# Kernel optimization log

Measured on AMD Instinct MI355X. Metric: run time of the kernel, lower is better.

## Reference

```python
import jax, jax.numpy as jnp
import numpy as np

T, B, IN, HID, OUT = 100, 2048, 784, 100, 10
BETA = 0.9      # snn.Leaky(beta=0.9)
THRESH = 1.0    # snntorch default threshold
ALPHA = 2.0     # snntorch default ATan surrogate alpha

@jax.custom_vjp
def fire(x):
    # Heaviside spike with ATan surrogate gradient (snntorch default).
    return (x > 0).astype(x.dtype)

def _fire_fwd(x):
    return fire(x), x

def _fire_bwd(x, g):
    return (g * (ALPHA / 2) / (1 + (jnp.pi / 2 * ALPHA * x) ** 2),)

fire.defvjp(_fire_fwd, _fire_bwd)

def setup_inputs() -> dict:
    key = jax.random.key(0)
    k1, k2, k3 = jax.random.split(key, 3)
    x_seq = jax.random.normal(k1, (T, B, IN), dtype=jnp.float32)
    # nn.Linear weights are [out_features, in_features], bias=False
    w1 = jax.random.normal(k2, (HID, IN), dtype=jnp.float32) * (1.0 / np.sqrt(IN))
    w2 = jax.random.normal(k3, (OUT, HID), dtype=jnp.float32) * (1.0 / np.sqrt(HID))
    return {"x_seq": x_seq, "w1": w1, "w2": w2}

def _leaky_step(mem, cur):
    # snntorch Leaky, reset_mechanism='subtract':
    # reset = H(mem_prev - thresh) (detached); mem = beta*mem + input - reset*thresh; spk = fire(mem - thresh)
    reset = jax.lax.stop_gradient((mem > THRESH).astype(mem.dtype))
    mem = BETA * mem + cur - reset * THRESH
    spk = fire(mem - THRESH)
    return spk, mem

def reference(x_seq, w1, w2):
    batch = x_seq.shape[1]
    def step(carry, x_t):
        mem1, mem2 = carry
        spk1, mem1 = _leaky_step(mem1, x_t @ w1.T)      # [B,HID]
        spk2, mem2 = _leaky_step(mem2, spk1 @ w2.T)     # [B,OUT]
        return (mem1, mem2), spk2
    init = (jnp.zeros((batch, HID), x_seq.dtype),
            jnp.zeros((batch, OUT), x_seq.dtype))
    _, spk2_seq = jax.lax.scan(step, init, x_seq)
    return spk2_seq.sum(axis=0)  # spk2_sum: [B, OUT]
```

## Files before the change

### kernel.cpp

```cpp
#include <hip/hip_runtime.h>

#define T_STEPS 100
#define B_SZ    2048
#define IN_DIM  784
#define HID_DIM 100
#define OUT_DIM 10
#define BN      112
#define BMR     128
#define KC      16
#define NSTEP   (IN_DIM / KC)
#define LDP     144

typedef double f64x4 __attribute__((ext_vector_type(4)));
#define MFMA64(a, b, c) __builtin_amdgcn_mfma_f64_16x16x4f64((a), (b), (c), 0, 0, 0)

__global__ void pad_w1(const float* __restrict__ w1, float* __restrict__ w1p) {
  int i = blockIdx.x * 256 + threadIdx.x;
  if (i < BN * IN_DIM) w1p[i] = (i < HID_DIM * IN_DIM) ? w1[i] : 0.0f;
}

__global__ __launch_bounds__(256, 2)
void snn_gemm1(const float* __restrict__ x,
               const float* __restrict__ w1p,
               double* __restrict__ cur)
{
  const int tid  = threadIdx.x;
  const int lane = tid & 63;
  const int wv   = tid >> 6;
  const int kg   = lane >> 4;
  const int il   = lane & 15;
  const long rowBase = (long)blockIdx.x * BMR;

  __shared__ float xls[2][KC][LDP];
  __shared__ float wls[2][KC][LDP];

  const int  srow = tid >> 1;
  const int  skh  = (tid & 1) * 8;
  const float* xsrc = x   + (rowBase + srow) * (long)IN_DIM + skh;
  const float* wsrc = w1p + (long)srow * IN_DIM + skh;
  const bool   dow  = tid < 2 * BN;

  float4 xa, xb, wa, wb;
  auto LOAD = [&](int s) {
    const float4* xp = reinterpret_cast<const float4*>(xsrc + s * KC);
    xa = xp[0]; xb = xp[1];
    if (dow) {
      const float4* wp = reinterpret_cast<const float4*>(wsrc + s * KC);
      wa = wp[0]; wb = wp[1];
    }
  };
  auto STORE = [&](int buf) {
    xls[buf][skh + 0][srow] = xa.x; xls[buf][skh + 1][srow] = xa.y;
    xls[buf][skh + 2][srow] = xa.z; xls[buf][skh + 3][srow] = xa.w;
    xls[buf][skh + 4][srow] = xb.x; xls[buf][skh + 5][srow] = xb.y;
    xls[buf][skh + 6][srow] = xb.z; xls[buf][skh + 7][srow] = xb.w;
    if (dow) {
      wls[buf][skh + 0][srow] = wa.x; wls[buf][skh + 1][srow] = wa.y;
      wls[buf][skh + 2][srow] = wa.z; wls[buf][skh + 3][srow] = wa.w;
      wls[buf][skh + 4][srow] = wb.x; wls[buf][skh + 5][srow] = wb.y;
      wls[buf][skh + 6][srow] = wb.z; wls[buf][skh + 7][srow] = wb.w;
    }
  };

  LOAD(0);

  f64x4 z = {0.0, 0.0, 0.0, 0.0};
  const double eil = (double)il;
  const double d0 = (kg == 0) ? 1.0 : 0.0;
  const double d1 = (kg == 1) ? 1.0 : 0.0;
  const double d2 = (kg == 2) ? 1.0 : 0.0;
  const double d3 = (kg == 3) ? 1.0 : 0.0;
  const f64x4 Prow0 = MFMA64(eil, d0, z);
  const f64x4 Prow1 = MFMA64(eil, d1, z);
  const f64x4 Pcol0 = MFMA64(d0, eil, z);
  const f64x4 Pcol1 = MFMA64(d1, eil, z);
  const f64x4 Pv0   = MFMA64(d0, d0, z);
  const f64x4 Pv1   = MFMA64(d1, d1, z);
  const f64x4 Pv2   = MFMA64(d2, d2, z);
  const f64x4 Pv3   = MFMA64(d3, d3, z);

  bool okl = true;
  int rowof[4], colof[4];
#pragma unroll
  for (int r = 0; r < 4; ++r) {
    okl = okl && (Pv0[r] == 1.0) && (Pv1[r] == 1.0) && (Pv2[r] == 1.0) && (Pv3[r] == 1.0);
    okl = okl && (Prow0[r] == Prow1[r]) && (Pcol0[r] == Pcol1[r]);
    const int rr = (int)Prow0[r];
    const int cc = (int)Pcol0[r];
    okl = okl && ((double)rr == Prow0[r]) && (rr >= 0) && (rr < 16);
    okl = okl && ((double)cc == Pcol0[r]) && (cc >= 0) && (cc < 16);
    rowof[r] = rr; colof[r] = cc;
  }
  if (__all(okl ? 1 : 0) == 0) {
#pragma unroll
    for (int r = 0; r < 4; ++r) { rowof[r] = kg * 4 + r; colof[r] = il; }
  }

  f64x4 acc[2][7];
#pragma unroll
  for (int rt = 0; rt < 2; ++rt)
#pragma unroll
    for (int ht = 0; ht < 7; ++ht) acc[rt][ht] = z;

  STORE(0); LOAD(1);
  __syncthreads();

#pragma unroll 1
  for (int s = 0; s < NSTEP; ++s) {
    if (s + 1 < NSTEP) STORE((s + 1) & 1);
    if (s + 2 < NSTEP) LOAD(s + 2);
    const int buf = s & 1;

#pragma unroll
    for (int kk = 0; kk < 4; ++kk) {
      const int kr = kk * 4 + kg;
      const double a0 = (double)xls[buf][kr][wv * 32 + il];
      const double a1 = (double)xls[buf][kr][wv * 32 + 16 + il];
      double b[7];
#pragma unroll
      for (int ht = 0; ht < 7; ++ht)
        b[ht] = (double)wls[buf][kr][ht * 16 + il];
#pragma unroll
      for (int ht = 0; ht < 7; ++ht) {
        acc[0][ht] = MFMA64(a0, b[ht], acc[0][ht]);
        acc[1][ht] = MFMA64(a1, b[ht], acc[1][ht]);
      }
    }
    __syncthreads();
  }

#pragma unroll
  for (int rt = 0; rt < 2; ++rt) {
    const long r0 = rowBase + wv * 32 + rt * 16;
#pragma unroll
    for (int ht = 0; ht < 7; ++ht)
#pragma unroll
      for (int m = 0; m < 4; ++m)
        cur[(r0 + rowof[m]) * BN + ht * 16 + colof[m]] = acc[rt][ht][m];
  }
}

__global__ __launch_bounds__(256)
void snn_recur(const double* __restrict__ cur,
               const float* __restrict__ w2,
               double* __restrict__ mem1s, float* __restrict__ spk1s,
               double* __restrict__ mem2s, float* __restrict__ spk2s,
               float* __restrict__ outs,
               float* __restrict__ dout,
               int chunkT, int isFirst, int isLast)
{
  const int tid = threadIdx.x;
  const int b0  = blockIdx.x * 8;
  __shared__ float w2l[OUT_DIM * HID_DIM];
  __shared__ float spkl[8 * BN];

  if (tid < 250)
    reinterpret_cast<float4*>(w2l)[tid] = reinterpret_cast<const float4*>(w2)[tid];

  const bool pa = tid < 224;
  const int  sl = tid / 28, q4 = (tid % 28) * 4;
  const long aOff = (long)(b0 + sl) * BN + q4;
  double m1[4] = {0.0, 0.0, 0.0, 0.0};
  float4 s1 = make_float4(0.f, 0.f, 0.f, 0.f);
  if (pa && !isFirst) {
    const double2* mp = reinterpret_cast<const double2*>(mem1s + aOff);
    double2 a = mp[0], b = mp[1];
    m1[0] = a.x; m1[1] = a.y; m1[2] = b.x; m1[3] = b.y;
    s1 = *reinterpret_cast<const float4*>(spk1s + aOff);
  }

  const bool pb = tid < 80;
  const int  ss = tid / 10, oo = tid % 10;
  const long bOff = (long)b0 * OUT_DIM + tid;
  double m2 = 0.0;
  float s2 = 0.f, oacc = 0.f;
  if (pb && !isFirst) { m2 = mem2s[bOff]; s2 = spk2s[bOff]; oacc = outs[bOff]; }

  __syncthreads();

  for (int tt = 0; tt < chunkT; ++tt) {
    if (pa) {
      const double2* cp = reinterpret_cast<const double2*>(
          cur + ((long)tt * B_SZ + b0 + sl) * BN + q4);
      const double2 ca = cp[0], cb = cp[1];
      double cu[4] = {ca.x, ca.y, cb.x, cb.y};
      float4 sp;
      float* spv = &sp.x;
      const float* s1v = &s1.x;
#pragma unroll
      for (int j = 0; j < 4; ++j) {
        double m = 0.9 * m1[j];
        m = m + cu[j];
        m = m - (double)s1v[j];
        spv[j] = (m > 1.0) ? 1.0f : 0.0f;
        m1[j] = m;
      }
      s1 = sp;
      *reinterpret_cast<float4*>(&spkl[sl * BN + q4]) = sp;
    }
    __syncthreads();
    if (pb) {
      const float* sr = &spkl[ss * BN];
      const float* wr = &w2l[oo * HID_DIM];
      double a0 = 0.0, a1 = 0.0, a2 = 0.0, a3 = 0.0;
#pragma unroll
      for (int h = 0; h < 100; h += 4) {
        a0 = fma((double)sr[h],     (double)wr[h],     a0);
        a1 = fma((double)sr[h + 1], (double)wr[h + 1], a1);
        a2 = fma((double)sr[h + 2], (double)wr[h + 2], a2);
        a3 = fma((double)sr[h + 3], (double)wr[h + 3], a3);
      }
      const double a = (a0 + a1) + (a2 + a3);
      double m = 0.9 * m2;
      m = m + a;
      m = m - (double)s2;
      const float sp = (m > 1.0) ? 1.0f : 0.0f;
      m2 = m; s2 = sp; oacc += sp;
    }
    __syncthreads();
  }

  if (pa) {
    double2* mp = reinterpret_cast<double2*>(mem1s + aOff);
    mp[0] = make_double2(m1[0], m1[1]);
    mp[1] = make_double2(m1[2], m1[3]);
    *reinterpret_cast<float4*>(spk1s + aOff) = s1;
  }
  if (pb) {
    mem2s[bOff] = m2; spk2s[bOff] = s2; outs[bOff] = oacc;
    if (isLast) dout[bOff] = oacc;
  }
}

extern "C" void kernel_launch(void* const* d_in, const int* in_sizes, int n_in,
                              void* d_out, int out_size, void* d_ws, size_t ws_size,
                              hipStream_t stream) {
  const float* x  = (const float*)d_in[0];
  const float* w1 = (const float*)d_in[1];
  const float* w2 = (const float*)d_in[2];
  float* out = (float*)d_out;

  char* ws = (char*)d_ws;
  float*  w1p   = (float*) (ws);
  double* mem1s = (double*)(ws +  351232);
  float*  spk1s = (float*) (ws + 2186240);
  double* mem2s = (double*)(ws + 3103744);
  float*  spk2s = (float*) (ws + 3267584);
  float*  outs  = (float*) (ws + 3349504);
  double* cur   = (double*)(ws + 3431424);

  pad_w1<<<dim3((BN * IN_DIM + 255) / 256), dim3(256), 0, stream>>>(w1, w1p);

  const size_t perT = (size_t)B_SZ * BN * 8;
  size_t curCap = ws_size > (size_t)3431424 ? ws_size - 3431424 : 0;
  int Tc = (int)(curCap / perT);
  if (Tc > T_STEPS) Tc = T_STEPS;
  if (Tc < 1) Tc = 1;

  for (int t0 = 0; t0 < T_STEPS; t0 += Tc) {
    const int ct = (T_STEPS - t0 < Tc) ? (T_STEPS - t0) : Tc;
    snn_gemm1<<<dim3(ct * (B_SZ / BMR)), dim3(256), 0, stream>>>(
        x + (size_t)t0 * B_SZ * IN_DIM, w1p, cur);
    snn_recur<<<dim3(B_SZ / 8), dim3(256), 0, stream>>>(
        cur, w2, mem1s, spk1s, mem2s, spk2s, outs, out,
        ct, (t0 == 0) ? 1 : 0, (t0 + ct >= T_STEPS) ? 1 : 0);
  }
}
```

Before: 809.9 us.

## Halve GEMM row tile, shrink recurrence blocks, prefetch cur and split layer-2 dot

The GEMM tile shrinks from 128 to 64 rows, so each wave holds one 16-row accumulator set, with tighter LDS padding and a launch bound of 3 waves per SIMD. This raises occupancy and the block count. The recurrence kernel now takes 4 batch rows per block, which doubles the grid. It prefetches the next timestep's cur values into registers and splits each layer-2 dot product across two lanes combined with a shuffle, shortening the serial per-step critical path. The cost is half the weight reuse per GEMM block and many idle threads in the 256-thread recurrence blocks.

```diff
diff --git a/kernel.cpp b/kernel.cpp
--- a/kernel.cpp
+++ b/kernel.cpp
@@ -6,10 +6,11 @@
 #define HID_DIM 100
 #define OUT_DIM 10
 #define BN      112
-#define BMR     128
+#define BMR     64
 #define KC      16
 #define NSTEP   (IN_DIM / KC)
-#define LDP     144
+#define XLP     80
+#define WLP     112
 
 typedef double f64x4 __attribute__((ext_vector_type(4)));
 #define MFMA64(a, b, c) __builtin_amdgcn_mfma_f64_16x16x4f64((a), (b), (c), 0, 0, 0)
@@ -19,7 +20,7 @@
   if (i < BN * IN_DIM) w1p[i] = (i < HID_DIM * IN_DIM) ? w1[i] : 0.0f;
 }
 
-__global__ __launch_bounds__(256, 2)
+__global__ __launch_bounds__(256, 3)
 void snn_gemm1(const float* __restrict__ x,
                const float* __restrict__ w1p,
                double* __restrict__ cur)
@@ -31,34 +32,33 @@
   const int il   = lane & 15;
   const long rowBase = (long)blockIdx.x * BMR;
 
-  __shared__ float xls[2][KC][LDP];
-  __shared__ float wls[2][KC][LDP];
-
-  const int  srow = tid >> 1;
+  __shared__ float xls[2][KC][XLP];
+  __shared__ float wls[2][KC][WLP];
+
+  const int xrow = tid >> 2;
+  const int xq   = (tid & 3) * 4;
+  const float* xsrc = x + (rowBase + xrow) * (long)IN_DIM + xq;
+  const int  wrow = tid >> 1;
   const int  skh  = (tid & 1) * 8;
-  const float* xsrc = x   + (rowBase + srow) * (long)IN_DIM + skh;
-  const float* wsrc = w1p + (long)srow * IN_DIM + skh;
+  const float* wsrc = w1p + (long)wrow * IN_DIM + skh;
   const bool   dow  = tid < 2 * BN;
 
-  float4 xa, xb, wa, wb;
+  float4 xg, wa, wb;
   auto LOAD = [&](int s) {
-    const float4* xp = reinterpret_cast<const float4*>(xsrc + s * KC);
-    xa = xp[0]; xb = xp[1];
+    xg = *reinterpret_cast<const float4*>(xsrc + s * KC);
     if (dow) {
       const float4* wp = reinterpret_cast<const float4*>(wsrc + s * KC);
       wa = wp[0]; wb = wp[1];
     }
   };
   auto STORE = [&](int buf) {
-    xls[buf][skh + 0][srow] = xa.x; xls[buf][skh + 1][srow] = xa.y;
-    xls[buf][skh + 2][srow] = xa.z; xls[buf][skh + 3][srow] = xa.w;
-    xls[buf][skh + 4][srow] = xb.x; xls[buf][skh + 5][srow] = xb.y;
-    xls[buf][skh + 6][srow] = xb.z; xls[buf][skh + 7][srow] = xb.w;
+    xls[buf][xq + 0][xrow] = xg.x; xls[buf][xq + 1][xrow] = xg.y;
+    xls[buf][xq + 2][xrow] = xg.z; xls[buf][xq + 3][xrow] = xg.w;
     if (dow) {
-      wls[buf][skh + 0][srow] = wa.x; wls[buf][skh + 1][srow] = wa.y;
-      wls[buf][skh + 2][srow] = wa.z; wls[buf][skh + 3][srow] = wa.w;
-      wls[buf][skh + 4][srow] = wb.x; wls[buf][skh + 5][srow] = wb.y;
-      wls[buf][skh + 6][srow] = wb.z; wls[buf][skh + 7][srow] = wb.w;
+      wls[buf][skh + 0][wrow] = wa.x; wls[buf][skh + 1][wrow] = wa.y;
+      wls[buf][skh + 2][wrow] = wa.z; wls[buf][skh + 3][wrow] = wa.w;
+      wls[buf][skh + 4][wrow] = wb.x; wls[buf][skh + 5][wrow] = wb.y;
+      wls[buf][skh + 6][wrow] = wb.z; wls[buf][skh + 7][wrow] = wb.w;
     }
   };
 
@@ -96,11 +96,9 @@
     for (int r = 0; r < 4; ++r) { rowof[r] = kg * 4 + r; colof[r] = il; }
   }
 
-  f64x4 acc[2][7];
-#pragma unroll
-  for (int rt = 0; rt < 2; ++rt)
-#pragma unroll
-    for (int ht = 0; ht < 7; ++ht) acc[rt][ht] = z;
+  f64x4 acc[7];
+#pragma unroll
+  for (int ht = 0; ht < 7; ++ht) acc[ht] = z;
 
   STORE(0); LOAD(1);
   __syncthreads();
@@ -114,30 +112,24 @@
 #pragma unroll
     for (int kk = 0; kk < 4; ++kk) {
       const int kr = kk * 4 + kg;
-      const double a0 = (double)xls[buf][kr][wv * 32 + il];
-      const double a1 = (double)xls[buf][kr][wv * 32 + 16 + il];
+      const double a0 = (double)xls[buf][kr][wv * 16 + il];
       double b[7];
 #pragma unroll
       for (int ht = 0; ht < 7; ++ht)
         b[ht] = (double)wls[buf][kr][ht * 16 + il];
 #pragma unroll
-      for (int ht = 0; ht < 7; ++ht) {
-        acc[0][ht] = MFMA64(a0, b[ht], acc[0][ht]);
-        acc[1][ht] = MFMA64(a1, b[ht], acc[1][ht]);
-      }
+      for (int ht = 0; ht < 7; ++ht)
+        acc[ht] = MFMA64(a0, b[ht], acc[ht]);
     }
     __syncthreads();
   }
 
-#pragma unroll
-  for (int rt = 0; rt < 2; ++rt) {
-    const long r0 = rowBase + wv * 32 + rt * 16;
-#pragma unroll
-    for (int ht = 0; ht < 7; ++ht)
-#pragma unroll
-      for (int m = 0; m < 4; ++m)
-        cur[(r0 + rowof[m]) * BN + ht * 16 + colof[m]] = acc[rt][ht][m];
-  }
+  const long r0 = rowBase + wv * 16;
+#pragma unroll
+  for (int ht = 0; ht < 7; ++ht)
+#pragma unroll
+    for (int m = 0; m < 4; ++m)
+      cur[(r0 + rowof[m]) * BN + ht * 16 + colof[m]] = acc[ht][m];
 }
 
 __global__ __launch_bounds__(256)
@@ -150,14 +142,14 @@
                int chunkT, int isFirst, int isLast)
 {
   const int tid = threadIdx.x;
-  const int b0  = blockIdx.x * 8;
+  const int b0  = blockIdx.x * 4;
   __shared__ float w2l[OUT_DIM * HID_DIM];
-  __shared__ float spkl[8 * BN];
+  __shared__ float spkl[4 * BN];
 
   if (tid < 250)
     reinterpret_cast<float4*>(w2l)[tid] = reinterpret_cast<const float4*>(w2)[tid];
 
-  const bool pa = tid < 224;
+  const bool pa = tid < 112;
   const int  sl = tid / 28, q4 = (tid % 28) * 4;
   const long aOff = (long)(b0 + sl) * BN + q4;
   double m1[4] = {0.0, 0.0, 0.0, 0.0};
@@ -170,20 +162,29 @@
   }
 
   const bool pb = tid < 80;
-  const int  ss = tid / 10, oo = tid % 10;
-  const long bOff = (long)b0 * OUT_DIM + tid;
+  const int  pp = tid >> 1, hf = tid & 1;
+  const int  ss = pp / 10, oo = pp % 10;
+  const long bOff = (long)b0 * OUT_DIM + pp;
   double m2 = 0.0;
   float s2 = 0.f, oacc = 0.f;
-  if (pb && !isFirst) { m2 = mem2s[bOff]; s2 = spk2s[bOff]; oacc = outs[bOff]; }
+  if (pb && !isFirst && hf == 0) { m2 = mem2s[bOff]; s2 = spk2s[bOff]; oacc = outs[bOff]; }
 
   __syncthreads();
+
+  double2 ca, cb;
+  if (pa) {
+    const double2* cp = reinterpret_cast<const double2*>(cur + (long)b0 * BN + sl * BN + q4);
+    ca = cp[0]; cb = cp[1];
+  }
 
   for (int tt = 0; tt < chunkT; ++tt) {
     if (pa) {
+      double cu[4] = {ca.x, ca.y, cb.x, cb.y};
+      const int tn = (tt + 1 < chunkT) ? tt + 1 : tt;
       const double2* cp = reinterpret_cast<const double2*>(
-          cur + ((long)tt * B_SZ + b0 + sl) * BN + q4);
-      const double2 ca = cp[0], cb = cp[1];
-      double cu[4] = {ca.x, ca.y, cb.x, cb.y};
+          cur + ((long)tn * B_SZ + b0 + sl) * BN + q4);
+      ca = cp[0]; cb = cp[1];
+
       float4 sp;
       float* spv = &sp.x;
       const float* s1v = &s1.x;
@@ -200,22 +201,23 @@
     }
     __syncthreads();
     if (pb) {
-      const float* sr = &spkl[ss * BN];
-      const float* wr = &w2l[oo * HID_DIM];
-      double a0 = 0.0, a1 = 0.0, a2 = 0.0, a3 = 0.0;
-#pragma unroll
-      for (int h = 0; h < 100; h += 4) {
+      const float* sr = &spkl[ss * BN] + hf * 50;
+      const float* wr = &w2l[oo * HID_DIM] + hf * 50;
+      double a0 = 0.0, a1 = 0.0;
+#pragma unroll
+      for (int h = 0; h < 50; h += 2) {
         a0 = fma((double)sr[h],     (double)wr[h],     a0);
         a1 = fma((double)sr[h + 1], (double)wr[h + 1], a1);
-        a2 = fma((double)sr[h + 2], (double)wr[h + 2], a2);
-        a3 = fma((double)sr[h + 3], (double)wr[h + 3], a3);
       }
-      const double a = (a0 + a1) + (a2 + a3);
-      double m = 0.9 * m2;
-      m = m + a;
-      m = m - (double)s2;
-      const float sp = (m > 1.0) ? 1.0f : 0.0f;
-      m2 = m; s2 = sp; oacc += sp;
+      double a = a0 + a1;
+      a = a + __shfl_xor(a, 1);
+      if (hf == 0) {
+        double m = 0.9 * m2;
+        m = m + a;
+        m = m - (double)s2;
+        const float sp = (m > 1.0) ? 1.0f : 0.0f;
+        m2 = m; s2 = sp; oacc += sp;
+      }
     }
     __syncthreads();
   }
@@ -226,7 +228,7 @@
     mp[1] = make_double2(m1[2], m1[3]);
     *reinterpret_cast<float4*>(spk1s + aOff) = s1;
   }
-  if (pb) {
+  if (pb && hf == 0) {
     mem2s[bOff] = m2; spk2s[bOff] = s2; outs[bOff] = oacc;
     if (isLast) dout[bOff] = oacc;
   }
@@ -261,7 +263,7 @@
     const int ct = (T_STEPS - t0 < Tc) ? (T_STEPS - t0) : Tc;
     snn_gemm1<<<dim3(ct * (B_SZ / BMR)), dim3(256), 0, stream>>>(
         x + (size_t)t0 * B_SZ * IN_DIM, w1p, cur);
-    snn_recur<<<dim3(B_SZ / 8), dim3(256), 0, stream>>>(
+    snn_recur<<<dim3(B_SZ / 4), dim3(256), 0, stream>>>(
         cur, w2, mem1s, spk1s, mem2s, spk2s, outs, out,
         ct, (t0 == 0) ? 1 : 0, (t0 + ct >= T_STEPS) ? 1 : 0);
   }
```

After: 720.7 us. -11.0%, faster.
